# Kernel optimization log

Hardware: AMD Instinct MI355X
Metric: run time of the kernel (lower is better)

## Reference

```python
import jax, jax.numpy as jnp
import numpy as np

ALPHA = 2.0  # spikingjelly default ATan surrogate alpha
EPS = 1e-5   # BatchNorm eps

@jax.custom_vjp
def heaviside_atan(x):
    return (x >= 0.0).astype(x.dtype)

def _ha_fwd(x):
    return heaviside_atan(x), x

def _ha_bwd(x, g):
    return (g * ALPHA / (2.0 * (1.0 + (jnp.pi / 2.0 * ALPHA * x) ** 2)),)

heaviside_atan.defvjp(_ha_fwd, _ha_bwd)

def lif(x_seq, tau=2.0, v_th=1.0):
    # MultiStepLIFNode, v_reset=0 (hard reset), detach_reset=True
    def step(v, x):
        v = v + (x - v) / tau
        s = heaviside_atan(v - v_th)
        v = v * (1.0 - jax.lax.stop_gradient(s))
        return v, s
    _, spikes = jax.lax.scan(step, jnp.zeros_like(x_seq[0]), x_seq)
    return spikes

def conv_bn(y, Wt, g, b):
    # 1x1 conv (no bias) + BatchNorm2d in training mode over flattened (T*B, H, W)
    y = jnp.einsum('tbchw,oc->tbohw', y, Wt)
    m = y.mean(axis=(0, 1, 3, 4), keepdims=True)
    v = y.var(axis=(0, 1, 3, 4), keepdims=True)
    C = Wt.shape[0]
    return (y - m) / jnp.sqrt(v + EPS) * g.reshape(1, 1, C, 1, 1) + b.reshape(1, 1, C, 1, 1)

def setup_inputs() -> dict:
    key = jax.random.key(0)
    ks = jax.random.split(key, 5)
    T, B, C, H, W = 4, 64, 384, 14, 14
    x = jax.random.normal(ks[0], (T, B, C, H, W), dtype=jnp.float32)
    Wq = jax.random.normal(ks[1], (C, C), dtype=jnp.float32) * 0.02
    Wk = jax.random.normal(ks[2], (C, C), dtype=jnp.float32) * 0.02
    Wv = jax.random.normal(ks[3], (C, C), dtype=jnp.float32) * 0.02
    Wp = jax.random.normal(ks[4], (C, C), dtype=jnp.float32) * 0.02
    ones = jnp.ones((C,), jnp.float32)
    zeros = jnp.zeros((C,), jnp.float32)
    return {"x": x, "Wq": Wq, "Wk": Wk, "Wv": Wv, "Wp": Wp,
            "gq": ones, "bq": zeros, "gk": ones, "bk": zeros,
            "gv": ones, "bv": zeros, "gp": ones, "bp": zeros}

def reference(x, Wq, Wk, Wv, Wp, gq, bq, gk, bk, gv, bv, gp, bp):
    T, B, C, H, W = x.shape
    nh = 8
    dh = C // nh
    N = H * W

    xs = lif(x)  # pre_lif

    def heads(y):  # [T,B,C,H,W] -> [T,B,h,N,dh]
        y = y.reshape(T, B, C, N).transpose(0, 1, 3, 2)
        return y.reshape(T, B, N, nh, dh).transpose(0, 1, 3, 2, 4)

    q = heads(lif(conv_bn(xs, Wq, gq, bq)))
    k = heads(lif(conv_bn(xs, Wk, gk, bk)))
    v = heads(lif(conv_bn(xs, Wv, gv, bv)))

    attn = jnp.einsum('tbhnd,tbhmd->tbhnm', q, k)      # no softmax
    o = jnp.einsum('tbhnm,tbhmd->tbhnd', attn, v) * 0.125
    o = o.transpose(0, 1, 2, 4, 3).reshape(T, B, C, N).reshape(T, B, C, H, W)
    o = lif(o, v_th=0.5)                                # attn_lif
    return conv_bn(o, Wp, gp, bp)                       # proj (no lif)
```

## Files before the change

kernel.cpp:

```cpp
#include <hip/hip_runtime.h>
#include <hip/hip_bf16.h>
#include <stdint.h>

#define T_  4
#define B_  64
#define C_  384
#define N_  196
#define NH  8
#define DH  48
#define TB_ (T_*B_)
#define R_  (T_*B_*N_)
#define NW  12
#define P_  12544
#define NCH 66
#define KG_ 17

typedef float f32x2 __attribute__((ext_vector_type(2)));

__global__ void transpose_w4(const float* __restrict__ s0, const float* __restrict__ s1,
                             const float* __restrict__ s2, const float* __restrict__ s3,
                             float* __restrict__ dst){
    int m = blockIdx.y;
    const float* src = (m==0)?s0:(m==1)?s1:(m==2)?s2:s3;
    int idx = blockIdx.x*256 + threadIdx.x;
    if (idx >= C_*C_) return;
    int o = idx % C_, c = idx / C_;
    dst[(size_t)m*C_*C_ + idx] = src[o*C_ + c];
}

__global__ __launch_bounds__(256) void pre_lif(const float* __restrict__ x,
                                               uint32_t* __restrict__ maskXS){
    int b = blockIdx.x / NW;
    int w = blockIdx.x % NW;
    int n = threadIdx.x;
    if (n >= N_) return;
    float v[32];
#pragma unroll
    for (int j=0;j<32;j++) v[j] = 0.f;
#pragma unroll
    for (int t=0;t<T_;t++){
        uint32_t word = 0;
#pragma unroll
        for (int j=0;j<32;j++){
            int c = w*32 + j;
            float xv = x[((size_t)(t*B_+b)*C_ + c)*N_ + n];
            v[j] = v[j] + (xv - v[j])*0.5f;
            if (v[j] >= 1.0f){ word |= (1u<<j); v[j] = 0.f; }
        }
        maskXS[((size_t)(t*B_+b)*N_ + n)*NW + w] = word;
    }
}

__global__ __launch_bounds__(256) void bit_transpose(const uint32_t* __restrict__ mask,
                                                     unsigned long long* __restrict__ maskT){
    int gw = blockIdx.x*4 + (threadIdx.x>>6);
    int lane = threadIdx.x & 63;
    int kc = gw/12, kw = gw%12;
    uint32_t mwv[12];
#pragma unroll
    for (int w=0;w<12;w++) mwv[w]=0u;
    if (gw < 784){
        int pix = gw*64 + lane;
        const uint4* m4 = (const uint4*)(mask + (size_t)pix*NW);
        uint4 a=m4[0], b=m4[1], c=m4[2];
        mwv[0]=a.x; mwv[1]=a.y; mwv[2]=a.z; mwv[3]=a.w;
        mwv[4]=b.x; mwv[5]=b.y; mwv[6]=b.z; mwv[7]=b.w;
        mwv[8]=c.x; mwv[9]=c.y; mwv[10]=c.z; mwv[11]=c.w;
    }
#pragma unroll
    for (int w=0; w<12; w++){
        uint32_t word = mwv[w];
#pragma unroll
        for (int j=0; j<32; j++){
            unsigned long long bal = __ballot((int)((word>>j)&1u));
            if (lane == 0)
                maskT[((size_t)kc*C_ + (w*32+j))*12 + kw] = bal;
        }
    }
}

__global__ __launch_bounds__(256) void gram(const unsigned long long* __restrict__ maskT,
                                            unsigned int* __restrict__ Gu){
    __shared__ unsigned int tile[64][49];
    int tid = threadIdx.x, wave = tid>>6, lane = tid&63;
    int kg = blockIdx.x, rg = blockIdx.y, cg = blockIdx.z;
    for (int i=tid; i<64*49; i+=256) ((unsigned int*)tile)[i] = 0u;
    __syncthreads();
    int kc = kg*4 + wave;
    if (kc < NCH){
        const uint4* rp = (const uint4*)(maskT + ((size_t)kc*C_ + rg*64 + lane)*12);
        uint32_t row[24];
#pragma unroll
        for (int q=0;q<6;q++){
            uint4 a = rp[q];
            row[4*q]=a.x; row[4*q+1]=a.y; row[4*q+2]=a.z; row[4*q+3]=a.w;
        }
        for (int cc=0; cc<48; cc++){
            const uint4* cp = (const uint4*)(maskT + ((size_t)kc*C_ + cg*48 + cc)*12);
            uint32_t col[24];
#pragma unroll
            for (int q=0;q<6;q++){
                uint4 a = cp[q];
                col[4*q]=a.x; col[4*q+1]=a.y; col[4*q+2]=a.z; col[4*q+3]=a.w;
            }
            unsigned int s = 0;
#pragma unroll
            for (int q=0;q<24;q++) s += (unsigned int)__popc(row[q]&col[q]);
            atomicAdd(&tile[lane][cc], s);
        }
    }
    __syncthreads();
    for (int i=tid; i<64*48; i+=256){
        int r = i/48, cc = i%48;
        unsigned int v = tile[r][cc];
        if (v) atomicAdd(&Gu[(size_t)(rg*64+r)*C_ + cg*48 + cc], v);
    }
}

__global__ __launch_bounds__(384) void bn_from_gram(const unsigned int* __restrict__ Gu,
        const float* __restrict__ WTall,
        const float* __restrict__ g0, const float* __restrict__ b0,
        const float* __restrict__ g1, const float* __restrict__ b1,
        const float* __restrict__ g2, const float* __restrict__ b2,
        float* __restrict__ scaleOut, float* __restrict__ shiftOut, int wtBase){
    __shared__ float w4[384][4];
    __shared__ float sred[8][6];
    int t = threadIdx.x, wave = t>>6, lane = t&63;
    int br = blockIdx.y;
    const float* WT = WTall + (size_t)(wtBase+br)*C_*C_;
    int o0 = blockIdx.x*4;
    float4 wv = *(const float4*)(WT + (size_t)t*C_ + o0);
    w4[t][0]=wv.x; w4[t][1]=wv.y; w4[t][2]=wv.z; w4[t][3]=wv.w;
    __syncthreads();
    float h0=0.f,h1=0.f,h2=0.f,h3=0.f;
#pragma unroll 4
    for (int c=0;c<C_;c++){
        float gv = (float)Gu[(size_t)c*C_ + t];
        float4 wc = *(const float4*)&w4[c][0];
        h0 += gv*wc.x; h1 += gv*wc.y; h2 += gv*wc.z; h3 += gv*wc.w;
    }
    float cnt = (float)Gu[(size_t)t*C_ + t];
    float p0=wv.x*h0, p1=wv.y*h1, p2=wv.z*h2, p3=wv.w*h3;
    float q0=cnt*wv.x, q1=cnt*wv.y, q2=cnt*wv.z, q3=cnt*wv.w;
#pragma unroll
    for (int off=32; off>0; off>>=1){
        p0+=__shfl_down(p0,off); p1+=__shfl_down(p1,off);
        p2+=__shfl_down(p2,off); p3+=__shfl_down(p3,off);
        q0+=__shfl_down(q0,off); q1+=__shfl_down(q1,off);
        q2+=__shfl_down(q2,off); q3+=__shfl_down(q3,off);
    }
    if (lane == 0){
        sred[0][wave]=p0; sred[1][wave]=p1; sred[2][wave]=p2; sred[3][wave]=p3;
        sred[4][wave]=q0; sred[5][wave]=q1; sred[6][wave]=q2; sred[7][wave]=q3;
    }
    __syncthreads();
    if (t < 4){
        const float* g  = (br==0)?g0:(br==1)?g1:g2;
        const float* bb = (br==0)?b0:(br==1)?b1:b2;
        float ss = ((sred[t][0]+sred[t][1])+(sred[t][2]+sred[t][3]))+(sred[t][4]+sred[t][5]);
        float sm = ((sred[4+t][0]+sred[4+t][1])+(sred[4+t][2]+sred[4+t][3]))+(sred[4+t][4]+sred[4+t][5]);
        float m   = sm / (float)R_;
        float var = ss / (float)R_ - m*m;
        float sc  = g[o0+t] / sqrtf(var + 1e-5f);
        scaleOut[br*C_ + o0+t] = sc;
        shiftOut[br*C_ + o0+t] = bb[o0+t] - m*sc;
    }
}

__global__ __launch_bounds__(256) void conv_lif3(const uint32_t* __restrict__ mask,
        const float* __restrict__ WTall,
        const float* __restrict__ scaleAll, const float* __restrict__ shiftAll,
        uint32_t* __restrict__ moQ, uint32_t* __restrict__ moK, uint32_t* __restrict__ moV){
    __shared__ uint16_t lst[4][416];
    __shared__ float scLDS[3*C_];
    __shared__ float shLDS[3*C_];
    int tid = threadIdx.x, wave = tid>>6, lane = tid&63;
    int pix0 = blockIdx.x*4 + wave;
    for (int i=tid; i<3*C_; i+=256){ scLDS[i]=scaleAll[i]; shLDS[i]=shiftAll[i]; }
    __syncthreads();

    float v0[6]={0,0,0,0,0,0}, v1[6]={0,0,0,0,0,0}, v2[6]={0,0,0,0,0,0};
    for (int t=0;t<T_;t++){
        size_t pix = (size_t)t*P_ + pix0;
        const uint4* m4 = (const uint4*)(mask + pix*NW);
        uint4 ma = m4[0], mb = m4[1], mc = m4[2];
        uint32_t mwv[12] = {ma.x,ma.y,ma.z,ma.w, mb.x,mb.y,mb.z,mb.w, mc.x,mc.y,mc.z,mc.w};
        int cnt = 0;
#pragma unroll
        for (int w=0;w<12;w++) cnt += __popc(mwv[w]);
        if (lane < 12){
            int off = 0;
            uint32_t mybits = 0;
#pragma unroll
            for (int w=0;w<12;w++){
                if (w < lane) off += __popc(mwv[w]);
                if (w == lane) mybits = mwv[w];
            }
            while (mybits){
                lst[wave][off++] = (uint16_t)((lane<<5) + __builtin_ctz(mybits));
                mybits &= mybits - 1;
            }
        }
        __syncthreads();

#pragma unroll
        for (int br=0; br<3; ++br){
            const float* WT = WTall + (size_t)br*C_*C_ + lane;
            float ya[6]={0,0,0,0,0,0}, yb[6]={0,0,0,0,0,0};
            float yc[6]={0,0,0,0,0,0}, yd[6]={0,0,0,0,0,0};
            int i = 0;
            for (; i+3 < cnt; i += 4){
                ushort4 cs = *(const ushort4*)&lst[wave][i];
                const float* q0 = WT + (size_t)cs.x*C_;
                const float* q1 = WT + (size_t)cs.y*C_;
                const float* q2 = WT + (size_t)cs.z*C_;
                const float* q3 = WT + (size_t)cs.w*C_;
#pragma unroll
                for (int j=0;j<6;j++){
                    ya[j] += q0[j<<6]; yb[j] += q1[j<<6];
                    yc[j] += q2[j<<6]; yd[j] += q3[j<<6];
                }
            }
            for (; i < cnt; ++i){
                int c = lst[wave][i];
                const float* q0 = WT + (size_t)c*C_;
#pragma unroll
                for (int j=0;j<6;j++) ya[j] += q0[j<<6];
            }
            float* vs = (br==0)?v0:(br==1)?v1:v2;
            uint32_t words[12];
#pragma unroll
            for (int j=0;j<6;j++){
                int o = (j<<6) + lane;
                float val = ((ya[j]+yb[j])+(yc[j]+yd[j]))*scLDS[br*C_+o] + shLDS[br*C_+o];
                float vv = vs[j];
                vv = vv + (val - vv)*0.5f;
                int s = (vv >= 1.0f);
                unsigned long long bal = __ballot(s);
                if (s) vv = 0.f;
                vs[j] = vv;
                words[2*j]   = (uint32_t)bal;
                words[2*j+1] = (uint32_t)(bal>>32);
            }
            if (lane == 0){
                uint32_t* mo = (br==0)?moQ:(br==1)?moK:moV;
                uint4* o4 = (uint4*)(mo + pix*NW);
                o4[0] = make_uint4(words[0],words[1],words[2],words[3]);
                o4[1] = make_uint4(words[4],words[5],words[6],words[7]);
                o4[2] = make_uint4(words[8],words[9],words[10],words[11]);
            }
        }
        __syncthreads();
    }
}

__global__ __launch_bounds__(256) void attention_lif(const uint32_t* __restrict__ mq,
                                                     const uint32_t* __restrict__ mk,
                                                     const uint32_t* __restrict__ mv,
                                                     uint16_t* __restrict__ mo){
    __shared__ unsigned long long kT[DH][4];
    __shared__ unsigned long long vT[DH][4];
    __shared__ uint32_t Cp[DH*25];

    int h = blockIdx.x & 7;
    int b = blockIdx.x >> 3;
    int tid = threadIdx.x, wv = tid>>6, lane = tid&63;
    int sw  = (h*DH) >> 5;
    int shf = (h*DH) & 31;

    float vm[DH];
#pragma unroll
    for (int d=0;d<DH;d++) vm[d] = 0.f;

    for (int t=0;t<T_;t++){
        int tb = t*B_ + b;
        unsigned long long q = 0, kk = 0, vvv = 0;
        if (tid < N_){
            const uint32_t* pq = mq + ((size_t)tb*N_ + tid)*NW + sw;
            const uint32_t* pk = mk + ((size_t)tb*N_ + tid)*NW + sw;
            const uint32_t* pv = mv + ((size_t)tb*N_ + tid)*NW + sw;
            unsigned long long lo, hi;
            lo = pq[0]; hi = pq[1];
            q   = (shf ? ((lo>>16) | (hi<<16)) : (lo | (hi<<32))) & 0xFFFFFFFFFFFFULL;
            lo = pk[0]; hi = pk[1];
            kk  = (shf ? ((lo>>16) | (hi<<16)) : (lo | (hi<<32))) & 0xFFFFFFFFFFFFULL;
            lo = pv[0]; hi = pv[1];
            vvv = (shf ? ((lo>>16) | (hi<<16)) : (lo | (hi<<32))) & 0xFFFFFFFFFFFFULL;
        }
#pragma unroll 1
        for (int d=0; d<DH; d++){
            unsigned long long bk_ = __ballot((int)((kk >>d)&1ull));
            unsigned long long bv_ = __ballot((int)((vvv>>d)&1ull));
            if (lane == 0){ kT[d][wv] = bk_; vT[d][wv] = bv_; }
        }
        __syncthreads();

        if (tid < 240){
            int j  = tid / 5;
            int dg = tid % 5;
            int d0 = dg*10;
            int d1 = (dg==4) ? 48 : d0+10;
            unsigned long long ka=kT[j][0], kb=kT[j][1], kc=kT[j][2], kd=kT[j][3];
            for (int d=d0; d<d1; d+=2){
                uint32_t c0 = (uint32_t)(__popcll(ka&vT[d][0]) + __popcll(kb&vT[d][1])
                            + __popcll(kc&vT[d][2]) + __popcll(kd&vT[d][3]));
                uint32_t c1 = (uint32_t)(__popcll(ka&vT[d+1][0]) + __popcll(kb&vT[d+1][1])
                            + __popcll(kc&vT[d+1][2]) + __popcll(kd&vT[d+1][3]));
                Cp[j*25 + (d>>1)] = c0 | (c1<<16);
            }
        }
        __syncthreads();

        if (tid < N_){
            uint32_t acc[24];
#pragma unroll
            for (int p=0;p<24;p++) acc[p] = 0u;
            unsigned long long qb = q;
            while (qb){
                int j = __builtin_ctzll(qb); qb &= qb-1;
                const uint32_t* row = &Cp[j*25];
#pragma unroll
                for (int p=0;p<24;p++) acc[p] += row[p];
            }
            unsigned long long sp = 0;
#pragma unroll
            for (int d=0; d<DH; d++){
                uint32_t a = (d&1) ? (acc[d>>1]>>16) : (acc[d>>1]&0xFFFFu);
                float o = 0.125f*(float)a;
                vm[d] = vm[d] + (o - vm[d])*0.5f;
                if (vm[d] >= 0.5f){ sp |= (1ull<<d); vm[d] = 0.f; }
            }
            size_t rec = ((size_t)tb*N_ + tid)*24 + 3*h;
            mo[rec]   = (uint16_t)(sp);
            mo[rec+1] = (uint16_t)(sp >> 16);
            mo[rec+2] = (uint16_t)(sp >> 32);
        }
        __syncthreads();
    }
}

__global__ __launch_bounds__(256) void proj_out(const uint32_t* __restrict__ mask,
                                                const float* __restrict__ WT,
                                                const float* __restrict__ scale,
                                                const float* __restrict__ shift,
                                                float* __restrict__ out){
    __shared__ float tile[192][49];
    __shared__ uint16_t lst[4][392];
    int bid = blockIdx.x;
    int tb = bid>>3, r7 = bid&7, nq = r7>>1, ch = r7&1;
    int n0 = nq*49, c0 = ch*192;
    int tid = threadIdx.x, wave = tid>>6, lane = tid&63;
    float sc[3], sh[3];
#pragma unroll
    for (int i=0;i<3;i++){
        sc[i] = scale[c0+(i<<6)+lane];
        sh[i] = shift[c0+(i<<6)+lane];
    }
    for (int p=wave; p<49; p+=4){
        size_t pix = (size_t)tb*N_ + n0 + p;
        const uint4* m4 = (const uint4*)(mask + pix*NW);
        uint4 ma = m4[0], mb = m4[1], mc = m4[2];
        uint32_t mwv[12] = {ma.x,ma.y,ma.z,ma.w, mb.x,mb.y,mb.z,mb.w, mc.x,mc.y,mc.z,mc.w};
        int cnt = 0;
#pragma unroll
        for (int w=0;w<12;w++) cnt += __popc(mwv[w]);
        if (lane < 12){
            int off = 0;
            uint32_t mybits = 0;
#pragma unroll
            for (int w=0;w<12;w++){
                if (w < lane) off += __popc(mwv[w]);
                if (w == lane) mybits = mwv[w];
            }
            while (mybits){
                lst[wave][off++] = (uint16_t)((lane<<5) + __builtin_ctz(mybits));
                mybits &= mybits - 1;
            }
        }
        float ya[3]={0,0,0}, yb[3]={0,0,0}, yc[3]={0,0,0}, yd[3]={0,0,0};
        int i = 0;
        for (; i+3 < cnt; i += 4){
            ushort4 cs = *(const ushort4*)&lst[wave][i];
            const float* q0 = WT + (size_t)cs.x*C_ + c0 + lane;
            const float* q1 = WT + (size_t)cs.y*C_ + c0 + lane;
            const float* q2 = WT + (size_t)cs.z*C_ + c0 + lane;
            const float* q3 = WT + (size_t)cs.w*C_ + c0 + lane;
#pragma unroll
            for (int j=0;j<3;j++){
                ya[j] += q0[j<<6]; yb[j] += q1[j<<6];
                yc[j] += q2[j<<6]; yd[j] += q3[j<<6];
            }
        }
        for (; i < cnt; ++i){
            int c = lst[wave][i];
            const float* q0 = WT + (size_t)c*C_ + c0 + lane;
#pragma unroll
            for (int j=0;j<3;j++) ya[j] += q0[j<<6];
        }
#pragma unroll
        for (int j=0;j<3;j++)
            tile[(j<<6)+lane][p] = ((ya[j]+yb[j])+(yc[j]+yd[j]))*sc[j] + sh[j];
    }
    __syncthreads();
    for (int r=wave; r<192; r+=4){
        if (lane < 49)
            out[((size_t)tb*C_ + c0 + r)*N_ + n0 + lane] = tile[r][lane];
    }
}

extern "C" void kernel_launch(void* const* d_in, const int* in_sizes, int n_in,
                              void* d_out, int out_size, void* d_ws, size_t ws_size,
                              hipStream_t stream) {
    const float* x  = (const float*)d_in[0];
    const float* Wq = (const float*)d_in[1];
    const float* Wk = (const float*)d_in[2];
    const float* Wv = (const float*)d_in[3];
    const float* Wp = (const float*)d_in[4];
    const float* gq = (const float*)d_in[5];
    const float* bq = (const float*)d_in[6];
    const float* gk = (const float*)d_in[7];
    const float* bk = (const float*)d_in[8];
    const float* gv = (const float*)d_in[9];
    const float* bv = (const float*)d_in[10];
    const float* gp = (const float*)d_in[11];
    const float* bp = (const float*)d_in[12];

    char* w = (char*)d_ws;
    size_t off = 0;
    uint32_t* maskXS = (uint32_t*)(w + off); off += (size_t)R_*NW*4;
    uint32_t* maskQ  = (uint32_t*)(w + off); off += (size_t)R_*NW*4;
    uint32_t* maskK  = (uint32_t*)(w + off); off += (size_t)R_*NW*4;
    uint32_t* maskV  = (uint32_t*)(w + off); off += (size_t)R_*NW*4;
    float* WTall = (float*)(w + off); off += (size_t)4*C_*C_*4;
    unsigned long long* maskT = (unsigned long long*)(w + off); off += (size_t)NCH*C_*12*8;
    unsigned int* Gu = (unsigned int*)(w + off); off += (size_t)C_*C_*4;
    float* scaleB = (float*)(w + off); off += (size_t)4*C_*4;
    float* shiftB = (float*)(w + off); off += (size_t)4*C_*4;
    uint32_t* maskOL = maskXS;

    transpose_w4<<<dim3((C_*C_+255)/256, 4),256,0,stream>>>(Wq, Wk, Wv, Wp, WTall);

    pre_lif<<<B_*NW,256,0,stream>>>(x, maskXS);

    hipMemsetAsync(Gu, 0, (size_t)C_*C_*4, stream);
    bit_transpose<<<198,256,0,stream>>>(maskXS, maskT);
    gram<<<dim3(KG_,6,8),256,0,stream>>>(maskT, Gu);
    bn_from_gram<<<dim3(96,3),384,0,stream>>>(Gu, WTall, gq,bq, gk,bk, gv,bv,
                                              scaleB, shiftB, 0);

    conv_lif3<<<P_/4,256,0,stream>>>(maskXS, WTall, scaleB, shiftB,
                                     maskQ, maskK, maskV);

    attention_lif<<<B_*NH,256,0,stream>>>(maskQ, maskK, maskV, (uint16_t*)maskOL);

    hipMemsetAsync(Gu, 0, (size_t)C_*C_*4, stream);
    bit_transpose<<<198,256,0,stream>>>(maskOL, maskT);
    gram<<<dim3(KG_,6,8),256,0,stream>>>(maskT, Gu);
    bn_from_gram<<<dim3(96,1),384,0,stream>>>(Gu, WTall, gp,bp, gp,bp, gp,bp,
                                              scaleB + 3*C_, shiftB + 3*C_, 3);

    proj_out<<<TB_*8,256,0,stream>>>(maskOL, WTall + (size_t)3*C_*C_,
                                     scaleB + 3*C_, shiftB + 3*C_, (float*)d_out);
}
```

Baseline: 402.9 us.

## Split attention over T, fuse bit-transposes into LIF kernels, tile weight transpose

Attention is split into attn_O, parallel over all T*B*heads with no serial loop over time, which writes per-pixel count tensors, and a separate attn_lif kernel that runs the membrane recurrence over T. The bit-transpose for the Gram BN statistics is fused into pre_lif and attn_lif, which removes the separate bit_transpose kernels. The transposed masks and Gram buffers are split so that a single memset clears them. The weight transpose now goes through shared-memory tiles. This adds a large intermediate count buffer (R*8*24 words) in global memory. pre_lif's chunk layout uses 86 chunks with partial words, which relies on the zeroing.

```diff
diff --git a/kernel.cpp b/kernel.cpp
--- a/kernel.cpp
+++ b/kernel.cpp
@@ -12,66 +12,52 @@
 #define R_  (T_*B_*N_)
 #define NW  12
 #define P_  12544
-#define NCH 66
-#define KG_ 17
+#define NCHX 86
+#define NCHO 66
 
 typedef float f32x2 __attribute__((ext_vector_type(2)));
 
-__global__ void transpose_w4(const float* __restrict__ s0, const float* __restrict__ s1,
-                             const float* __restrict__ s2, const float* __restrict__ s3,
-                             float* __restrict__ dst){
-    int m = blockIdx.y;
+__global__ __launch_bounds__(256) void transpose_w4(const float* __restrict__ s0,
+        const float* __restrict__ s1, const float* __restrict__ s2,
+        const float* __restrict__ s3, float* __restrict__ dst){
+    __shared__ float tile[64][65];
+    int m = blockIdx.z;
     const float* src = (m==0)?s0:(m==1)?s1:(m==2)?s2:s3;
-    int idx = blockIdx.x*256 + threadIdx.x;
-    if (idx >= C_*C_) return;
-    int o = idx % C_, c = idx / C_;
-    dst[(size_t)m*C_*C_ + idx] = src[o*C_ + c];
+    int o0 = blockIdx.x*64, c0 = blockIdx.y*64;
+    int lane = threadIdx.x & 63, w = threadIdx.x >> 6;
+    for (int r = w; r < 64; r += 4)
+        tile[r][lane] = src[(size_t)(o0+r)*C_ + c0 + lane];
+    __syncthreads();
+    for (int r = w; r < 64; r += 4)
+        dst[(size_t)m*C_*C_ + (size_t)(c0+r)*C_ + o0 + lane] = tile[lane][r];
 }
 
 __global__ __launch_bounds__(256) void pre_lif(const float* __restrict__ x,
-                                               uint32_t* __restrict__ maskXS){
+                                               uint32_t* __restrict__ maskXS,
+                                               unsigned long long* __restrict__ maskT){
     int b = blockIdx.x / NW;
     int w = blockIdx.x % NW;
     int n = threadIdx.x;
     if (n >= N_) return;
+    int wv = n >> 6, lane = n & 63;
     float v[32];
 #pragma unroll
     for (int j=0;j<32;j++) v[j] = 0.f;
 #pragma unroll
     for (int t=0;t<T_;t++){
+        int tb = t*B_ + b;
         uint32_t word = 0;
 #pragma unroll
         for (int j=0;j<32;j++){
             int c = w*32 + j;
-            float xv = x[((size_t)(t*B_+b)*C_ + c)*N_ + n];
+            float xv = x[((size_t)tb*C_ + c)*N_ + n];
             v[j] = v[j] + (xv - v[j])*0.5f;
             if (v[j] >= 1.0f){ word |= (1u<<j); v[j] = 0.f; }
         }
-        maskXS[((size_t)(t*B_+b)*N_ + n)*NW + w] = word;
-    }
-}
-
-__global__ __launch_bounds__(256) void bit_transpose(const uint32_t* __restrict__ mask,
-                                                     unsigned long long* __restrict__ maskT){
-    int gw = blockIdx.x*4 + (threadIdx.x>>6);
-    int lane = threadIdx.x & 63;
-    int kc = gw/12, kw = gw%12;
-    uint32_t mwv[12];
-#pragma unroll
-    for (int w=0;w<12;w++) mwv[w]=0u;
-    if (gw < 784){
-        int pix = gw*64 + lane;
-        const uint4* m4 = (const uint4*)(mask + (size_t)pix*NW);
-        uint4 a=m4[0], b=m4[1], c=m4[2];
-        mwv[0]=a.x; mwv[1]=a.y; mwv[2]=a.z; mwv[3]=a.w;
-        mwv[4]=b.x; mwv[5]=b.y; mwv[6]=b.z; mwv[7]=b.w;
-        mwv[8]=c.x; mwv[9]=c.y; mwv[10]=c.z; mwv[11]=c.w;
-    }
-#pragma unroll
-    for (int w=0; w<12; w++){
-        uint32_t word = mwv[w];
-#pragma unroll
-        for (int j=0; j<32; j++){
+        maskXS[((size_t)tb*N_ + n)*NW + w] = word;
+        int g = tb*4 + wv, kc = g/12, kw = g - kc*12;
+#pragma unroll
+        for (int j=0;j<32;j++){
             unsigned long long bal = __ballot((int)((word>>j)&1u));
             if (lane == 0)
                 maskT[((size_t)kc*C_ + (w*32+j))*12 + kw] = bal;
@@ -80,14 +66,14 @@
 }
 
 __global__ __launch_bounds__(256) void gram(const unsigned long long* __restrict__ maskT,
-                                            unsigned int* __restrict__ Gu){
+                                            unsigned int* __restrict__ Gu, int nch){
     __shared__ unsigned int tile[64][49];
     int tid = threadIdx.x, wave = tid>>6, lane = tid&63;
     int kg = blockIdx.x, rg = blockIdx.y, cg = blockIdx.z;
     for (int i=tid; i<64*49; i+=256) ((unsigned int*)tile)[i] = 0u;
     __syncthreads();
     int kc = kg*4 + wave;
-    if (kc < NCH){
+    if (kc < nch){
         const uint4* rp = (const uint4*)(maskT + ((size_t)kc*C_ + rg*64 + lane)*12);
         uint32_t row[24];
 #pragma unroll
@@ -254,88 +240,113 @@
     }
 }
 
-__global__ __launch_bounds__(256) void attention_lif(const uint32_t* __restrict__ mq,
-                                                     const uint32_t* __restrict__ mk,
-                                                     const uint32_t* __restrict__ mv,
-                                                     uint16_t* __restrict__ mo){
+__global__ __launch_bounds__(256) void attn_O(const uint32_t* __restrict__ mq,
+                                              const uint32_t* __restrict__ mk,
+                                              const uint32_t* __restrict__ mv,
+                                              uint32_t* __restrict__ aCnt){
     __shared__ unsigned long long kT[DH][4];
     __shared__ unsigned long long vT[DH][4];
     __shared__ uint32_t Cp[DH*25];
 
-    int h = blockIdx.x & 7;
-    int b = blockIdx.x >> 3;
+    int h  = blockIdx.x & 7;
+    int tb = blockIdx.x >> 3;
     int tid = threadIdx.x, wv = tid>>6, lane = tid&63;
     int sw  = (h*DH) >> 5;
     int shf = (h*DH) & 31;
 
-    float vm[DH];
-#pragma unroll
-    for (int d=0;d<DH;d++) vm[d] = 0.f;
-
+    unsigned long long q = 0, kk = 0, vvv = 0;
+    if (tid < N_){
+        const uint32_t* pq = mq + ((size_t)tb*N_ + tid)*NW + sw;
+        const uint32_t* pk = mk + ((size_t)tb*N_ + tid)*NW + sw;
+        const uint32_t* pv = mv + ((size_t)tb*N_ + tid)*NW + sw;
+        unsigned long long lo, hi;
+        lo = pq[0]; hi = pq[1];
+        q   = (shf ? ((lo>>16) | (hi<<16)) : (lo | (hi<<32))) & 0xFFFFFFFFFFFFULL;
+        lo = pk[0]; hi = pk[1];
+        kk  = (shf ? ((lo>>16) | (hi<<16)) : (lo | (hi<<32))) & 0xFFFFFFFFFFFFULL;
+        lo = pv[0]; hi = pv[1];
+        vvv = (shf ? ((lo>>16) | (hi<<16)) : (lo | (hi<<32))) & 0xFFFFFFFFFFFFULL;
+    }
+#pragma unroll 1
+    for (int d=0; d<DH; d++){
+        unsigned long long bk_ = __ballot((int)((kk >>d)&1ull));
+        unsigned long long bv_ = __ballot((int)((vvv>>d)&1ull));
+        if (lane == 0){ kT[d][wv] = bk_; vT[d][wv] = bv_; }
+    }
+    __syncthreads();
+
+    if (tid < 240){
+        int j  = tid / 5;
+        int dg = tid % 5;
+        int d0 = dg*10;
+        int d1 = (dg==4) ? 48 : d0+10;
+        unsigned long long ka=kT[j][0], kb=kT[j][1], kc=kT[j][2], kd=kT[j][3];
+        for (int d=d0; d<d1; d+=2){
+            uint32_t c0 = (uint32_t)(__popcll(ka&vT[d][0]) + __popcll(kb&vT[d][1])
+                        + __popcll(kc&vT[d][2]) + __popcll(kd&vT[d][3]));
+            uint32_t c1 = (uint32_t)(__popcll(ka&vT[d+1][0]) + __popcll(kb&vT[d+1][1])
+                        + __popcll(kc&vT[d+1][2]) + __popcll(kd&vT[d+1][3]));
+            Cp[j*25 + (d>>1)] = c0 | (c1<<16);
+        }
+    }
+    __syncthreads();
+
+    if (tid < N_){
+        uint32_t acc[24];
+#pragma unroll
+        for (int p=0;p<24;p++) acc[p] = 0u;
+        unsigned long long qb = q;
+        while (qb){
+            int j = __builtin_ctzll(qb); qb &= qb-1;
+            const uint32_t* row = &Cp[j*25];
+#pragma unroll
+            for (int p=0;p<24;p++) acc[p] += row[p];
+        }
+        uint4* ap = (uint4*)(aCnt + (((size_t)tb*NH + h)*N_ + tid)*24);
+        ap[0] = make_uint4(acc[0], acc[1], acc[2], acc[3]);
+        ap[1] = make_uint4(acc[4], acc[5], acc[6], acc[7]);
+        ap[2] = make_uint4(acc[8], acc[9], acc[10],acc[11]);
+        ap[3] = make_uint4(acc[12],acc[13],acc[14],acc[15]);
+        ap[4] = make_uint4(acc[16],acc[17],acc[18],acc[19]);
+        ap[5] = make_uint4(acc[20],acc[21],acc[22],acc[23]);
+    }
+}
+
+__global__ __launch_bounds__(64) void attn_lif(const uint32_t* __restrict__ aCnt,
+                                               uint16_t* __restrict__ mo,
+                                               unsigned long long* __restrict__ maskT){
+    int pg  = blockIdx.x;
+    int c16 = blockIdx.y;
+    int lane = threadIdx.x;
+    int pix0 = pg*64 + lane;
+    int b = pix0 / N_;
+    int n = pix0 - b*N_;
+    int h = c16 / 3, sub = c16 - h*3;
+    float vm[16];
+#pragma unroll
+    for (int cc=0;cc<16;cc++) vm[cc] = 0.f;
+#pragma unroll
     for (int t=0;t<T_;t++){
         int tb = t*B_ + b;
-        unsigned long long q = 0, kk = 0, vvv = 0;
-        if (tid < N_){
-            const uint32_t* pq = mq + ((size_t)tb*N_ + tid)*NW + sw;
-            const uint32_t* pk = mk + ((size_t)tb*N_ + tid)*NW + sw;
-            const uint32_t* pv = mv + ((size_t)tb*N_ + tid)*NW + sw;
-            unsigned long long lo, hi;
-            lo = pq[0]; hi = pq[1];
-            q   = (shf ? ((lo>>16) | (hi<<16)) : (lo | (hi<<32))) & 0xFFFFFFFFFFFFULL;
-            lo = pk[0]; hi = pk[1];
-            kk  = (shf ? ((lo>>16) | (hi<<16)) : (lo | (hi<<32))) & 0xFFFFFFFFFFFFULL;
-            lo = pv[0]; hi = pv[1];
-            vvv = (shf ? ((lo>>16) | (hi<<16)) : (lo | (hi<<32))) & 0xFFFFFFFFFFFFULL;
-        }
-#pragma unroll 1
-        for (int d=0; d<DH; d++){
-            unsigned long long bk_ = __ballot((int)((kk >>d)&1ull));
-            unsigned long long bv_ = __ballot((int)((vvv>>d)&1ull));
-            if (lane == 0){ kT[d][wv] = bk_; vT[d][wv] = bv_; }
-        }
-        __syncthreads();
-
-        if (tid < 240){
-            int j  = tid / 5;
-            int dg = tid % 5;
-            int d0 = dg*10;
-            int d1 = (dg==4) ? 48 : d0+10;
-            unsigned long long ka=kT[j][0], kb=kT[j][1], kc=kT[j][2], kd=kT[j][3];
-            for (int d=d0; d<d1; d+=2){
-                uint32_t c0 = (uint32_t)(__popcll(ka&vT[d][0]) + __popcll(kb&vT[d][1])
-                            + __popcll(kc&vT[d][2]) + __popcll(kd&vT[d][3]));
-                uint32_t c1 = (uint32_t)(__popcll(ka&vT[d+1][0]) + __popcll(kb&vT[d+1][1])
-                            + __popcll(kc&vT[d+1][2]) + __popcll(kd&vT[d+1][3]));
-                Cp[j*25 + (d>>1)] = c0 | (c1<<16);
-            }
-        }
-        __syncthreads();
-
-        if (tid < N_){
-            uint32_t acc[24];
-#pragma unroll
-            for (int p=0;p<24;p++) acc[p] = 0u;
-            unsigned long long qb = q;
-            while (qb){
-                int j = __builtin_ctzll(qb); qb &= qb-1;
-                const uint32_t* row = &Cp[j*25];
-#pragma unroll
-                for (int p=0;p<24;p++) acc[p] += row[p];
-            }
-            unsigned long long sp = 0;
-#pragma unroll
-            for (int d=0; d<DH; d++){
-                uint32_t a = (d&1) ? (acc[d>>1]>>16) : (acc[d>>1]&0xFFFFu);
-                float o = 0.125f*(float)a;
-                vm[d] = vm[d] + (o - vm[d])*0.5f;
-                if (vm[d] >= 0.5f){ sp |= (1ull<<d); vm[d] = 0.f; }
-            }
-            size_t rec = ((size_t)tb*N_ + tid)*24 + 3*h;
-            mo[rec]   = (uint16_t)(sp);
-            mo[rec+1] = (uint16_t)(sp >> 16);
-            mo[rec+2] = (uint16_t)(sp >> 32);
-        }
-        __syncthreads();
+        const uint4* ap = (const uint4*)(aCnt + (((size_t)tb*NH + h)*N_ + n)*24 + sub*8);
+        uint4 A = ap[0], Bv = ap[1];
+        uint32_t cw[8] = {A.x,A.y,A.z,A.w, Bv.x,Bv.y,Bv.z,Bv.w};
+        uint32_t bits = 0;
+#pragma unroll
+        for (int cc=0;cc<16;cc++){
+            uint32_t a = (cc&1) ? (cw[cc>>1]>>16) : (cw[cc>>1]&0xFFFFu);
+            float o = 0.125f*(float)a;
+            vm[cc] = vm[cc] + (o - vm[cc])*0.5f;
+            if (vm[cc] >= 0.5f){ bits |= (1u<<cc); vm[cc] = 0.f; }
+        }
+        mo[((size_t)t*P_ + pix0)*24 + c16] = (uint16_t)bits;
+        int g = t*196 + pg, kc = g/12, kw = g - kc*12;
+#pragma unroll
+        for (int cc=0;cc<16;cc++){
+            unsigned long long bal = __ballot((int)((bits>>cc)&1u));
+            if (lane == 0)
+                maskT[((size_t)kc*C_ + c16*16 + cc)*12 + kw] = bal;
+        }
     }
 }
 
@@ -432,31 +443,34 @@
     uint32_t* maskK  = (uint32_t*)(w + off); off += (size_t)R_*NW*4;
     uint32_t* maskV  = (uint32_t*)(w + off); off += (size_t)R_*NW*4;
     float* WTall = (float*)(w + off); off += (size_t)4*C_*C_*4;
-    unsigned long long* maskT = (unsigned long long*)(w + off); off += (size_t)NCH*C_*12*8;
-    unsigned int* Gu = (unsigned int*)(w + off); off += (size_t)C_*C_*4;
+    unsigned long long* maskTX = (unsigned long long*)(w + off); off += (size_t)NCHX*C_*12*8;
+    unsigned long long* maskTO = (unsigned long long*)(w + off); off += (size_t)NCHO*C_*12*8;
+    unsigned int* GuX = (unsigned int*)(w + off); off += (size_t)C_*C_*4;
+    unsigned int* GuO = (unsigned int*)(w + off); off += (size_t)C_*C_*4;
+    size_t zbytes = (size_t)NCHX*C_*12*8 + (size_t)NCHO*C_*12*8 + 2*(size_t)C_*C_*4;
+    uint32_t* aCnt = (uint32_t*)(w + off); off += (size_t)R_*NH*24*4;
     float* scaleB = (float*)(w + off); off += (size_t)4*C_*4;
     float* shiftB = (float*)(w + off); off += (size_t)4*C_*4;
     uint32_t* maskOL = maskXS;
 
-    transpose_w4<<<dim3((C_*C_+255)/256, 4),256,0,stream>>>(Wq, Wk, Wv, Wp, WTall);
-
-    pre_lif<<<B_*NW,256,0,stream>>>(x, maskXS);
-
-    hipMemsetAsync(Gu, 0, (size_t)C_*C_*4, stream);
-    bit_transpose<<<198,256,0,stream>>>(maskXS, maskT);
-    gram<<<dim3(KG_,6,8),256,0,stream>>>(maskT, Gu);
-    bn_from_gram<<<dim3(96,3),384,0,stream>>>(Gu, WTall, gq,bq, gk,bk, gv,bv,
+    hipMemsetAsync(maskTX, 0, zbytes, stream);
+
+    transpose_w4<<<dim3(6,6,4),256,0,stream>>>(Wq, Wk, Wv, Wp, WTall);
+
+    pre_lif<<<B_*NW,256,0,stream>>>(x, maskXS, maskTX);
+
+    gram<<<dim3((NCHX+3)/4,6,8),256,0,stream>>>(maskTX, GuX, NCHX);
+    bn_from_gram<<<dim3(96,3),384,0,stream>>>(GuX, WTall, gq,bq, gk,bk, gv,bv,
                                               scaleB, shiftB, 0);
 
     conv_lif3<<<P_/4,256,0,stream>>>(maskXS, WTall, scaleB, shiftB,
                                      maskQ, maskK, maskV);
 
-    attention_lif<<<B_*NH,256,0,stream>>>(maskQ, maskK, maskV, (uint16_t*)maskOL);
-
-    hipMemsetAsync(Gu, 0, (size_t)C_*C_*4, stream);
-    bit_transpose<<<198,256,0,stream>>>(maskOL, maskT);
-    gram<<<dim3(KG_,6,8),256,0,stream>>>(maskT, Gu);
-    bn_from_gram<<<dim3(96,1),384,0,stream>>>(Gu, WTall, gp,bp, gp,bp, gp,bp,
+    attn_O<<<TB_*NH,256,0,stream>>>(maskQ, maskK, maskV, aCnt);
+    attn_lif<<<dim3(196,24),64,0,stream>>>(aCnt, (uint16_t*)maskOL, maskTO);
+
+    gram<<<dim3((NCHO+3)/4,6,8),256,0,stream>>>(maskTO, GuO, NCHO);
+    bn_from_gram<<<dim3(96,1),384,0,stream>>>(GuO, WTall, gp,bp, gp,bp, gp,bp,
                                               scaleB + 3*C_, shiftB + 3*C_, 3);
 
     proj_out<<<TB_*8,256,0,stream>>>(maskOL, WTall + (size_t)3*C_*C_,
```

After: 376.5 us, median of 3. 1.07x faster.
